# Performance work log

Hardware: AMD Instinct MI355X
Metric: run time of the kernel (lower is better)

## Reference

```python
import jax, jax.numpy as jnp
import numpy as np

B, L, D_MODEL = 2, 1024, 512
N_LAYERS, D_STATE, D_CONV = 6, 16, 4
D_INNER = 2 * D_MODEL          # Mamba default expand=2
DT_RANK = (D_MODEL + 15) // 16  # ceil(d_model/16) = 32
EPS = 1.1920929e-07             # torch RMSNorm default eps (fp32 machine eps)


def rmsnorm(x, w):
    return x * jax.lax.rsqrt(jnp.mean(x * x, axis=-1, keepdims=True) + EPS) * w


def selective_scan(u, dt, A, Bm, Cm, Dv):
    # u, dt: (B,L,E); A: (E,N); Bm, Cm: (B,L,N); Dv: (E,)
    dA = jnp.exp(jnp.einsum('ble,en->blen', dt, A))    # discretized A (ZOH)
    dBu = jnp.einsum('ble,bln->blen', dt * u, Bm)      # discretized B * u (Euler)

    def step(h, inp):
        dA_t, dBu_t, C_t = inp
        h = dA_t * h + dBu_t                           # (B,E,N) state update
        y = jnp.einsum('ben,bn->be', h, C_t)
        return h, y

    h0 = jnp.zeros((u.shape[0], u.shape[2], A.shape[1]), u.dtype)
    _, ys = jax.lax.scan(step, h0,
                         (dA.transpose(1, 0, 2, 3), dBu.transpose(1, 0, 2, 3),
                          Cm.transpose(1, 0, 2)))
    return ys.transpose(1, 0, 2) + u * Dv


def mamba_block(x, p):
    xz = jnp.einsum('bld,ed->ble', x, p['in_proj_w'])  # (B,L,2E)
    xi, z = jnp.split(xz, 2, axis=-1)
    # causal depthwise conv1d (kernel D_CONV) + bias + SiLU
    xc = jnp.pad(xi.transpose(0, 2, 1), ((0, 0), (0, 0), (D_CONV - 1, 0)))
    xc = jax.lax.conv_general_dilated(xc, p['conv_w'][:, None, :], (1,), 'VALID',
                                      feature_group_count=D_INNER)
    xi = jax.nn.silu(xc.transpose(0, 2, 1) + p['conv_b'])
    dbc = jnp.einsum('ble,re->blr', xi, p['x_proj_w'])  # (B,L,R+2N)
    dt, Bm, Cm = jnp.split(dbc, [DT_RANK, DT_RANK + D_STATE], axis=-1)
    dt = jax.nn.softplus(jnp.einsum('blr,er->ble', dt, p['dt_w']) + p['dt_b'])
    y = selective_scan(xi, dt, -jnp.exp(p['A_log']), Bm, Cm, p['D'])
    y = y * jax.nn.silu(z)                              # gate branch
    return jnp.einsum('ble,de->bld', y, p['out_w'])


def setup_inputs() -> dict:
    key = jax.random.key(0)
    ks = jax.random.split(key, 8)
    s = 0.02
    return {
        'x': jax.random.normal(ks[0], (B, L, D_MODEL), jnp.float32),
        'position_embedding': jax.random.normal(ks[1], (B, L, D_MODEL), jnp.float32) * 0.02,
        'norm_w': jnp.ones((D_MODEL,), jnp.float32),
        'in_proj_w': jax.random.normal(ks[2], (N_LAYERS, 2 * D_INNER, D_MODEL), jnp.float32) * s,
        'conv_w': jax.random.normal(ks[3], (N_LAYERS, D_INNER, D_CONV), jnp.float32) * 0.2,
        'conv_b': jnp.zeros((N_LAYERS, D_INNER), jnp.float32),
        'x_proj_w': jax.random.normal(ks[4], (N_LAYERS, DT_RANK + 2 * D_STATE, D_INNER), jnp.float32) * s,
        'dt_w': jax.random.normal(ks[5], (N_LAYERS, D_INNER, DT_RANK), jnp.float32) * s,
        'dt_b': jnp.full((N_LAYERS, D_INNER), -4.6, jnp.float32),  # softplus(dt_b) ~ 0.01
        'A_log': jnp.broadcast_to(
            jnp.log(jnp.arange(1, D_STATE + 1, dtype=jnp.float32)),
            (N_LAYERS, D_INNER, D_STATE)) + jnp.zeros((N_LAYERS, D_INNER, D_STATE), jnp.float32),
        'D': jnp.ones((N_LAYERS, D_INNER), jnp.float32),
        'out_w': jax.random.normal(ks[6], (N_LAYERS, D_MODEL, D_INNER), jnp.float32) * s,
    }


def reference(x, position_embedding, norm_w, in_proj_w, conv_w, conv_b,
              x_proj_w, dt_w, dt_b, A_log, D, out_w):
    stacked = dict(in_proj_w=in_proj_w, conv_w=conv_w, conv_b=conv_b,
                   x_proj_w=x_proj_w, dt_w=dt_w, dt_b=dt_b,
                   A_log=A_log, D=D, out_w=out_w)

    def body(h, p):
        h = h + position_embedding          # added at the start of every layer
        h = mamba_block(rmsnorm(h, norm_w), p)  # NOTE: no residual, per source
        return h, None

    h, _ = jax.lax.scan(body, x, stacked)
    return h
```

## Files before the change

kernel.cpp:

```cpp
#include <hip/hip_runtime.h>
#include <hip/hip_bf16.h>


typedef __attribute__((ext_vector_type(8))) short bf16x8;
typedef __attribute__((ext_vector_type(4))) float f32x4;

__device__ __forceinline__ float bf2f(unsigned short u) {
    unsigned int x = ((unsigned int)u) << 16;
    return __builtin_bit_cast(float, x);
}
__device__ __forceinline__ unsigned short f2bf(float f) {
    __hip_bfloat16 h = __float2bfloat16(f);
    return __builtin_bit_cast(unsigned short, h);
}
__device__ __forceinline__ float ldin(const void* p, size_t i, int isbf) {
    return isbf ? bf2f(((const unsigned short*)p)[i]) : ((const float*)p)[i];
}
__device__ __forceinline__ float softplus_f(float x) {
    return (x > 20.f) ? x : log1pf(__expf(x));
}
__device__ __forceinline__ void split2(float x, unsigned short& h, unsigned short& l) {
    h = f2bf(x);
    l = f2bf(x - bf2f(h));
}

#define S1 (6*2048*512)
#define S2 (6*512*1024)
#define S3 (6*64*1024)
#define S4 (6*1024*32)
__global__ __launch_bounds__(256) void wsplit_all(
    const void* __restrict__ ipw, const void* __restrict__ ow,
    const void* __restrict__ xpw, const void* __restrict__ dtw,
    const void* __restrict__ Dw,
    unsigned short* __restrict__ h1, unsigned short* __restrict__ l1,
    unsigned short* __restrict__ h2, unsigned short* __restrict__ l2,
    unsigned short* __restrict__ h3, unsigned short* __restrict__ l3,
    unsigned short* __restrict__ h4, unsigned short* __restrict__ l4,
    int* __restrict__ flag)
{
    int g = blockIdx.x * 256 + threadIdx.x;
    const int isbf = (*(const unsigned int*)Dw == 0x3F800000u) ? 0 : 1;
    if (g == 0) *flag = isbf;
    const void* src; unsigned short *dh, *dl; int i;
    if (g < S1)                { src = ipw; dh = h1; dl = l1; i = g; }
    else if (g < S1+S2)        { src = ow;  dh = h2; dl = l2; i = g - S1; }
    else if (g < S1+S2+S3)     { src = xpw; dh = h3; dl = l3; i = g - S1 - S2; }
    else if (g < S1+S2+S3+S4)  { src = dtw; dh = h4; dl = l4; i = g - S1 - S2 - S3; }
    else return;
    unsigned short hh, ll;
    split2(ldin(src, i, isbf), hh, ll);
    dh[i] = hh; dl[i] = ll;
}

__global__ __launch_bounds__(256) void gemm128(
    const unsigned short* __restrict__ Ah, const unsigned short* __restrict__ Al,
    int lda,
    const unsigned short* __restrict__ Wh, const unsigned short* __restrict__ Wl,
    long woff,
    float* __restrict__ Cf, int N, int K)
{
    __shared__ __align__(16) unsigned short As[2][128][40];
    __shared__ __align__(16) unsigned short Ws[2][128][40];

    const int m0 = blockIdx.x * 128, n0 = blockIdx.y * 128;
    const int t = threadIdx.x, lane = t & 63, wave = t >> 6;
    const int wm = (wave & 1) * 64, wn = (wave >> 1) * 64;
    const int srow = t >> 1, scol = (t & 1) * 16;

    const unsigned short* ah = Ah + (size_t)(m0 + srow) * lda + scol;
    const unsigned short* al = Al + (size_t)(m0 + srow) * lda + scol;
    const unsigned short* wh = Wh + woff + (size_t)(n0 + srow) * K + scol;
    const unsigned short* wl = Wl + woff + (size_t)(n0 + srow) * K + scol;

    f32x4 acc[4][4] = {};
    const int fm = lane & 15, fk = (lane >> 4) * 8;

    uint4 r0, r1, r2, r3, r4, r5, r6, r7;
#define LD128(K0) do { \
        r0 = *(const uint4*)(ah + (K0));     r1 = *(const uint4*)(ah + (K0) + 8); \
        r2 = *(const uint4*)(al + (K0));     r3 = *(const uint4*)(al + (K0) + 8); \
        r4 = *(const uint4*)(wh + (K0));     r5 = *(const uint4*)(wh + (K0) + 8); \
        r6 = *(const uint4*)(wl + (K0));     r7 = *(const uint4*)(wl + (K0) + 8); \
    } while (0)
#define ST128() do { \
        *(uint4*)(&As[0][srow][scol])     = r0; *(uint4*)(&As[0][srow][scol + 8]) = r1; \
        *(uint4*)(&As[1][srow][scol])     = r2; *(uint4*)(&As[1][srow][scol + 8]) = r3; \
        *(uint4*)(&Ws[0][srow][scol])     = r4; *(uint4*)(&Ws[0][srow][scol + 8]) = r5; \
        *(uint4*)(&Ws[1][srow][scol])     = r6; *(uint4*)(&Ws[1][srow][scol + 8]) = r7; \
    } while (0)

    LD128(0);
    ST128();
    __syncthreads();

    for (int k0 = 0; k0 < K; k0 += 32) {
        const int more = (k0 + 32 < K);
        if (more) LD128(k0 + 32);

        bf16x8 a_h[4], a_l[4], w_h[4], w_l[4];
#pragma unroll
        for (int i = 0; i < 4; ++i) {
            a_h[i] = *(const bf16x8*)(&As[0][wm + i * 16 + fm][fk]);
            a_l[i] = *(const bf16x8*)(&As[1][wm + i * 16 + fm][fk]);
            w_h[i] = *(const bf16x8*)(&Ws[0][wn + i * 16 + fm][fk]);
            w_l[i] = *(const bf16x8*)(&Ws[1][wn + i * 16 + fm][fk]);
        }
#pragma unroll
        for (int mi = 0; mi < 4; ++mi)
#pragma unroll
            for (int ni = 0; ni < 4; ++ni) {
                acc[mi][ni] = __builtin_amdgcn_mfma_f32_16x16x32_bf16(
                    a_h[mi], w_h[ni], acc[mi][ni], 0, 0, 0);
                acc[mi][ni] = __builtin_amdgcn_mfma_f32_16x16x32_bf16(
                    a_h[mi], w_l[ni], acc[mi][ni], 0, 0, 0);
                acc[mi][ni] = __builtin_amdgcn_mfma_f32_16x16x32_bf16(
                    a_l[mi], w_h[ni], acc[mi][ni], 0, 0, 0);
            }

        if (more) {
            __syncthreads();
            ST128();
            __syncthreads();
        }
    }
#undef LD128
#undef ST128

    const int col = lane & 15, rb = (lane >> 4) * 4;
#pragma unroll
    for (int mi = 0; mi < 4; ++mi)
#pragma unroll
        for (int ni = 0; ni < 4; ++ni)
#pragma unroll
            for (int r = 0; r < 4; ++r) {
                int gm = m0 + wm + mi * 16 + rb + r;
                int gn = n0 + wn + ni * 16 + col;
                Cf[(size_t)gm * N + gn] = acc[mi][ni][r];
            }
}

template <int ACT>
__global__ __launch_bounds__(256) void gemm_hl(
    const unsigned short* __restrict__ Ah, const unsigned short* __restrict__ Al,
    int lda,
    const unsigned short* __restrict__ Wh, const unsigned short* __restrict__ Wl,
    long woff,
    float* __restrict__ Cf, long zstride,
    const void* __restrict__ bias, long boff, const int* __restrict__ flag,
    int N, int K, int Kc)
{
    const int isbf = *flag;
    __shared__ __align__(16) unsigned short As[2][64][40];
    __shared__ __align__(16) unsigned short Ws[2][64][40];

    const int m0 = blockIdx.x * 64, n0 = blockIdx.y * 64;
    const int kb = blockIdx.z * Kc;
    const int t = threadIdx.x;
    const int lane = t & 63, wave = t >> 6;
    const int wm = (wave & 1) * 32, wn = (wave >> 1) * 32;
    const int srow = t >> 2, scol = (t & 3) * 8;

    const unsigned short* ah = Ah + (size_t)(m0 + srow) * lda + scol;
    const unsigned short* al = Al + (size_t)(m0 + srow) * lda + scol;
    const unsigned short* wh = Wh + woff + (size_t)(n0 + srow) * K + scol;
    const unsigned short* wl = Wl + woff + (size_t)(n0 + srow) * K + scol;

    f32x4 acc[2][2] = {};

    uint4 r0, r1, r2, r3;
#define LD64(K0) do { \
        r0 = *(const uint4*)(ah + (K0)); \
        r1 = *(const uint4*)(al + (K0)); \
        r2 = *(const uint4*)(wh + (K0)); \
        r3 = *(const uint4*)(wl + (K0)); \
    } while (0)
#define ST64() do { \
        *(uint4*)(&As[0][srow][scol]) = r0; \
        *(uint4*)(&As[1][srow][scol]) = r1; \
        *(uint4*)(&Ws[0][srow][scol]) = r2; \
        *(uint4*)(&Ws[1][srow][scol]) = r3; \
    } while (0)

    LD64(kb);
    ST64();
    __syncthreads();

    for (int k0 = kb; k0 < kb + Kc; k0 += 32) {
        const int more = (k0 + 32 < kb + Kc);
        if (more) LD64(k0 + 32);

        const int fm = lane & 15, fk = (lane >> 4) * 8;
        bf16x8 a0h = *(const bf16x8*)(&As[0][wm + fm][fk]);
        bf16x8 a1h = *(const bf16x8*)(&As[0][wm + 16 + fm][fk]);
        bf16x8 w0h = *(const bf16x8*)(&Ws[0][wn + fm][fk]);
        bf16x8 w1h = *(const bf16x8*)(&Ws[0][wn + 16 + fm][fk]);
        bf16x8 a0l = *(const bf16x8*)(&As[1][wm + fm][fk]);
        bf16x8 a1l = *(const bf16x8*)(&As[1][wm + 16 + fm][fk]);
        bf16x8 w0l = *(const bf16x8*)(&Ws[1][wn + fm][fk]);
        bf16x8 w1l = *(const bf16x8*)(&Ws[1][wn + 16 + fm][fk]);

        acc[0][0] = __builtin_amdgcn_mfma_f32_16x16x32_bf16(a0h, w0h, acc[0][0], 0, 0, 0);
        acc[0][1] = __builtin_amdgcn_mfma_f32_16x16x32_bf16(a0h, w1h, acc[0][1], 0, 0, 0);
        acc[1][0] = __builtin_amdgcn_mfma_f32_16x16x32_bf16(a1h, w0h, acc[1][0], 0, 0, 0);
        acc[1][1] = __builtin_amdgcn_mfma_f32_16x16x32_bf16(a1h, w1h, acc[1][1], 0, 0, 0);
        acc[0][0] = __builtin_amdgcn_mfma_f32_16x16x32_bf16(a0h, w0l, acc[0][0], 0, 0, 0);
        acc[0][1] = __builtin_amdgcn_mfma_f32_16x16x32_bf16(a0h, w1l, acc[0][1], 0, 0, 0);
        acc[1][0] = __builtin_amdgcn_mfma_f32_16x16x32_bf16(a1h, w0l, acc[1][0], 0, 0, 0);
        acc[1][1] = __builtin_amdgcn_mfma_f32_16x16x32_bf16(a1h, w1l, acc[1][1], 0, 0, 0);
        acc[0][0] = __builtin_amdgcn_mfma_f32_16x16x32_bf16(a0l, w0h, acc[0][0], 0, 0, 0);
        acc[0][1] = __builtin_amdgcn_mfma_f32_16x16x32_bf16(a0l, w1h, acc[0][1], 0, 0, 0);
        acc[1][0] = __builtin_amdgcn_mfma_f32_16x16x32_bf16(a1l, w0h, acc[1][0], 0, 0, 0);
        acc[1][1] = __builtin_amdgcn_mfma_f32_16x16x32_bf16(a1l, w1h, acc[1][1], 0, 0, 0);

        if (more) {
            __syncthreads();
            ST64();
            __syncthreads();
        }
    }
#undef LD64
#undef ST64

    float* Cp = Cf + (size_t)blockIdx.z * zstride;
    const int col = lane & 15, rb = (lane >> 4) * 4;
#pragma unroll
    for (int mi = 0; mi < 2; ++mi)
#pragma unroll
        for (int ni = 0; ni < 2; ++ni)
#pragma unroll
            for (int r = 0; r < 4; ++r) {
                int gm = m0 + wm + mi * 16 + rb + r;
                int gn = n0 + wn + ni * 16 + col;
                float v = acc[mi][ni][r];
                if (bias) v += ldin(bias, boff + gn, isbf);
                if (ACT == 1) v = softplus_f(v);
                Cp[(size_t)gm * N + gn] = v;
            }
}

__global__ __launch_bounds__(256) void xp_reduce(
    const float* __restrict__ Pxp, float* __restrict__ dbc,
    unsigned short* __restrict__ dth, unsigned short* __restrict__ dtl)
{
    int g = blockIdx.x * 256 + threadIdx.x;
    float s = 0.f;
#pragma unroll
    for (int z = 0; z < 8; ++z) s += Pxp[(size_t)z * 131072 + g];
    dbc[g] = s;
    int n = g & 63, t = g >> 6;
    if (n < 32) {
        unsigned short hh, ll;
        split2(s, hh, ll);
        dth[t * 32 + n] = hh; dtl[t * 32 + n] = ll;
    }
}

__global__ __launch_bounds__(256) void rmsnorm_k(
    const void* __restrict__ hsrc, int hdyn, const void* __restrict__ pos,
    const void* __restrict__ nw, const int* __restrict__ flag,
    unsigned short* __restrict__ xnh, unsigned short* __restrict__ xnl)
{
    const int isbf = *flag;
    const int row = blockIdx.x;
    const int t = threadIdx.x;
    const size_t base = (size_t)row * 512;
    float h0 = hdyn ? ldin(hsrc, base + t, isbf)       : ((const float*)hsrc)[base + t];
    float h1 = hdyn ? ldin(hsrc, base + 256 + t, isbf) : ((const float*)hsrc)[base + 256 + t];
    float v0 = h0 + ldin(pos, base + t, isbf);
    float v1 = h1 + ldin(pos, base + 256 + t, isbf);
    float ss = v0 * v0 + v1 * v1;
#pragma unroll
    for (int o = 32; o; o >>= 1) ss += __shfl_xor(ss, o, 64);
    __shared__ float sw[4];
    if ((t & 63) == 0) sw[t >> 6] = ss;
    __syncthreads();
    float tot = sw[0] + sw[1] + sw[2] + sw[3];
    float sc = rsqrtf(tot * (1.0f / 512.0f) + 1.1920929e-07f);
    float o0 = v0 * sc * ldin(nw, t, isbf);
    float o1 = v1 * sc * ldin(nw, 256 + t, isbf);
    unsigned short hh, ll;
    split2(o0, hh, ll); xnh[base + t] = hh;       xnl[base + t] = ll;
    split2(o1, hh, ll); xnh[base + 256 + t] = hh; xnl[base + 256 + t] = ll;
}

__global__ __launch_bounds__(256) void conv_silu_k(
    const float* __restrict__ xz,
    const void* __restrict__ cw, long cwoff,
    const void* __restrict__ cb, long cboff,
    const int* __restrict__ flag,
    float* __restrict__ xi,
    unsigned short* __restrict__ xih, unsigned short* __restrict__ xil)
{
    const int isbf = *flag;
    int g = blockIdx.x * 256 + threadIdx.x;
    int e = g & 1023;
    int l = (g >> 10) & 1023;
    int b = g >> 20;
    float acc = ldin(cb, cboff + e, isbf);
#pragma unroll
    for (int k = 0; k < 4; ++k) {
        int ls = l - 3 + k;
        if (ls >= 0)
            acc += ldin(cw, cwoff + e * 4 + k, isbf) *
                   xz[((size_t)(b * 1024 + ls)) * 2048 + e];
    }
    acc = acc / (1.f + __expf(-acc));
    xi[g] = acc;
    unsigned short hh, ll;
    split2(acc, hh, ll);
    xih[g] = hh; xil[g] = ll;
}

#define CL 16
#define NCH 64

__global__ __launch_bounds__(256) void scan_stage1(
    const float* __restrict__ dtp, const float* __restrict__ u,
    const float* __restrict__ dbc,
    const void* __restrict__ alog, long aoff, const int* __restrict__ flag,
    float* __restrict__ P, float* __restrict__ S)
{
    const int isbf = *flag;
    int g = blockIdx.x * 256 + threadIdx.x;
    int e = g & 1023, c = (g >> 10) & (NCH - 1), b = g >> 16;
    int t0 = b * 1024 + c * CL;

    float dv[CL], uv[CL];
#pragma unroll
    for (int i = 0; i < CL; ++i) {
        dv[i] = dtp[(size_t)(t0 + i) * 1024 + e];
        uv[i] = u[(size_t)(t0 + i) * 1024 + e];
    }

    float Aen[16], Pn[16], Sn[16];
#pragma unroll
    for (int n = 0; n < 16; ++n) {
        Aen[n] = -__expf(ldin(alog, aoff + e * 16 + n, isbf));
        Pn[n] = 1.f; Sn[n] = 0.f;
    }
#pragma unroll
    for (int i = 0; i < CL; ++i) {
        float d = dv[i], du = d * uv[i];
        const float4* Bp = (const float4*)(dbc + (size_t)(t0 + i) * 64 + 32);
        float4 b0 = Bp[0], b1 = Bp[1], b2 = Bp[2], b3 = Bp[3];
        float Bt[16] = {b0.x,b0.y,b0.z,b0.w, b1.x,b1.y,b1.z,b1.w,
                        b2.x,b2.y,b2.z,b2.w, b3.x,b3.y,b3.z,b3.w};
#pragma unroll
        for (int n = 0; n < 16; ++n) {
            float a = __expf(d * Aen[n]);
            Sn[n] = a * Sn[n] + du * Bt[n];
            Pn[n] *= a;
        }
    }
    size_t ob = ((size_t)(b * NCH + c) * 16) * 1024 + e;
#pragma unroll
    for (int n = 0; n < 16; ++n) {
        P[ob + (size_t)n * 1024] = Pn[n];
        S[ob + (size_t)n * 1024] = Sn[n];
    }
}

__global__ __launch_bounds__(256) void scan_stage2(
    float* __restrict__ PH, const float* __restrict__ S)
{
    int g = blockIdx.x * 256 + threadIdx.x;
    int e = g & 1023, n = (g >> 10) & 15, b = g >> 14;
    float H = 0.f;
    for (int cb = 0; cb < NCH; cb += 8) {
        float p[8], s[8];
#pragma unroll
        for (int j = 0; j < 8; ++j) {
            size_t idx = ((size_t)(b * NCH + cb + j) * 16 + n) * 1024 + e;
            p[j] = PH[idx]; s[j] = S[idx];
        }
#pragma unroll
        for (int j = 0; j < 8; ++j) {
            size_t idx = ((size_t)(b * NCH + cb + j) * 16 + n) * 1024 + e;
            PH[idx] = H;
            H = p[j] * H + s[j];
        }
    }
}

__global__ __launch_bounds__(256) void scan_stage3(
    const float* __restrict__ dtp, const float* __restrict__ u,
    const float* __restrict__ dbc,
    const void* __restrict__ alog, long aoff,
    const void* __restrict__ Dv, long doff,
    const int* __restrict__ flag,
    const float* __restrict__ xz, const float* __restrict__ H0,
    unsigned short* __restrict__ yh, unsigned short* __restrict__ yl)
{
    const int isbf = *flag;
    int g = blockIdx.x * 256 + threadIdx.x;
    int e = g & 1023, c = (g >> 10) & (NCH - 1), b = g >> 16;
    int t0 = b * 1024 + c * CL;

    float dv[CL], uv[CL], zv[CL];
#pragma unroll
    for (int i = 0; i < CL; ++i) {
        dv[i] = dtp[(size_t)(t0 + i) * 1024 + e];
        uv[i] = u[(size_t)(t0 + i) * 1024 + e];
        zv[i] = xz[(size_t)(t0 + i) * 2048 + 1024 + e];
    }

    float Aen[16], h[16];
    size_t ob = ((size_t)(b * NCH + c) * 16) * 1024 + e;
#pragma unroll
    for (int n = 0; n < 16; ++n) {
        Aen[n] = -__expf(ldin(alog, aoff + e * 16 + n, isbf));
        h[n] = H0[ob + (size_t)n * 1024];
    }
    float De = ldin(Dv, doff + e, isbf);
#pragma unroll
    for (int i = 0; i < CL; ++i) {
        float d = dv[i], uu = uv[i], du = d * uu;
        const float4* Bp = (const float4*)(dbc + (size_t)(t0 + i) * 64 + 32);
        float4 b0 = Bp[0], b1 = Bp[1], b2 = Bp[2], b3 = Bp[3];
        float4 c0 = Bp[4], c1 = Bp[5], c2 = Bp[6], c3 = Bp[7];
        float Bt[16] = {b0.x,b0.y,b0.z,b0.w, b1.x,b1.y,b1.z,b1.w,
                        b2.x,b2.y,b2.z,b2.w, b3.x,b3.y,b3.z,b3.w};
        float Ct[16] = {c0.x,c0.y,c0.z,c0.w, c1.x,c1.y,c1.z,c1.w,
                        c2.x,c2.y,c2.z,c2.w, c3.x,c3.y,c3.z,c3.w};
        float y = 0.f;
#pragma unroll
        for (int n = 0; n < 16; ++n) {
            float a = __expf(d * Aen[n]);
            h[n] = a * h[n] + du * Bt[n];
            y += h[n] * Ct[n];
        }
        float sz = zv[i] / (1.f + __expf(-zv[i]));
        float yv = (y + uu * De) * sz;
        unsigned short hh, ll;
        split2(yv, hh, ll);
        yh[(size_t)(t0 + i) * 1024 + e] = hh;
        yl[(size_t)(t0 + i) * 1024 + e] = ll;
    }
}

extern "C" void kernel_launch(void* const* d_in, const int* in_sizes, int n_in,
                              void* d_out, int out_size, void* d_ws, size_t ws_size,
                              hipStream_t stream)
{
    const void* x    = d_in[0];
    const void* pos  = d_in[1];
    const void* nw   = d_in[2];
    const void* ipw  = d_in[3];
    const void* cw   = d_in[4];
    const void* cb   = d_in[5];
    const void* xpw  = d_in[6];
    const void* dtw  = d_in[7];
    const void* dtb  = d_in[8];
    const void* alog = d_in[9];
    const void* Dw   = d_in[10];
    const void* ow   = d_in[11];

    char* w = (char*)d_ws;
    auto take = [&](size_t bytes) { char* p = w; w += (bytes + 255) & ~255ull; return p; };

    float* h    = (float*)take(2048ull * 512 * 4);
    float* xz   = (float*)take(2048ull * 2048 * 4);
    float* xi   = (float*)take(2048ull * 1024 * 4);
    float* dtf  = (float*)take(2048ull * 1024 * 4);
    float* dbc  = (float*)take(2048ull * 64 * 4);
    float* P    = (float*)take(2ull * NCH * 16 * 1024 * 4);
    float* S    = (float*)take(2ull * NCH * 16 * 1024 * 4);
    float* Pxp  = (float*)take(8ull * 2048 * 64 * 4);
    unsigned short* xnh = (unsigned short*)take(2048ull * 512 * 2);
    unsigned short* xnl = (unsigned short*)take(2048ull * 512 * 2);
    unsigned short* xih = (unsigned short*)take(2048ull * 1024 * 2);
    unsigned short* xil = (unsigned short*)take(2048ull * 1024 * 2);
    unsigned short* yh  = (unsigned short*)take(2048ull * 1024 * 2);
    unsigned short* yl  = (unsigned short*)take(2048ull * 1024 * 2);
    unsigned short* dth = (unsigned short*)take(2048ull * 32 * 2);
    unsigned short* dtl = (unsigned short*)take(2048ull * 32 * 2);
    unsigned short* wip_h = (unsigned short*)take(6ull * 2048 * 512 * 2);
    unsigned short* wip_l = (unsigned short*)take(6ull * 2048 * 512 * 2);
    unsigned short* wow_h = (unsigned short*)take(6ull * 512 * 1024 * 2);
    unsigned short* wow_l = (unsigned short*)take(6ull * 512 * 1024 * 2);
    unsigned short* wxp_h = (unsigned short*)take(6ull * 64 * 1024 * 2);
    unsigned short* wxp_l = (unsigned short*)take(6ull * 64 * 1024 * 2);
    unsigned short* wdt_h = (unsigned short*)take(6ull * 1024 * 32 * 2);
    unsigned short* wdt_l = (unsigned short*)take(6ull * 1024 * 32 * 2);
    int* flag = (int*)take(256);

    wsplit_all<<<(S1 + S2 + S3 + S4 + 255) / 256, 256, 0, stream>>>(
        ipw, ow, xpw, dtw, Dw,
        wip_h, wip_l, wow_h, wow_l, wxp_h, wxp_l, wdt_h, wdt_l, flag);

    for (int l = 0; l < 6; ++l) {
        rmsnorm_k<<<2048, 256, 0, stream>>>(
            l == 0 ? x : (const void*)h, l == 0 ? 1 : 0, pos, nw, flag, xnh, xnl);
        gemm128<<<dim3(16, 16), 256, 0, stream>>>(
            xnh, xnl, 512, wip_h, wip_l, (long)l * 2048 * 512, xz, 2048, 512);
        conv_silu_k<<<8192, 256, 0, stream>>>(xz, cw, (long)l * 4096, cb, (long)l * 1024,
                                              flag, xi, xih, xil);
        gemm_hl<0><<<dim3(32, 1, 8), 256, 0, stream>>>(
            xih, xil, 1024, wxp_h, wxp_l, (long)l * 64 * 1024,
            Pxp, 2048l * 64, nullptr, 0, flag, 64, 1024, 128);
        xp_reduce<<<512, 256, 0, stream>>>(Pxp, dbc, dth, dtl);
        gemm_hl<1><<<dim3(32, 16), 256, 0, stream>>>(
            dth, dtl, 32, wdt_h, wdt_l, (long)l * 1024 * 32,
            dtf, 0, dtb, (long)l * 1024, flag, 1024, 32, 32);
        scan_stage1<<<512, 256, 0, stream>>>(dtf, xi, dbc, alog, (long)l * 16384,
                                             flag, P, S);
        scan_stage2<<<128, 256, 0, stream>>>(P, S);
        scan_stage3<<<512, 256, 0, stream>>>(dtf, xi, dbc, alog, (long)l * 16384,
                                             Dw, (long)l * 1024, flag, xz, P, yh, yl);
        float* outp = (l < 5) ? h : (float*)d_out;
        gemm_hl<0><<<dim3(32, 8), 256, 0, stream>>>(
            yh, yl, 1024, wow_h, wow_l, (long)l * 512 * 1024,
            outp, 0, nullptr, 0, flag, 512, 1024, 1024);
    }
}
```

Before: 845.2 us.

## Fuse x_proj reduction, dt projection and scan stage1; derive chunk decay from dt sum

Merges the split-K reduction of x_proj, the dt_proj GEMM with softplus, and the first chunked-scan stage into one kernel. The 32-wide dt projection is now computed in fp32 from shared memory, so the bf16 hi/lo split of dt weights and the separate GEMM launch go away. Stage1 no longer writes the per-chunk decay product P. It stores the chunk sum of dt instead, and stage2 recomputes the decay as exp(A*sum dt), which cuts global traffic. The cost is redundant reduction work across the four e-groups and an extra exp per element in stage2.

Measured after the change: 835.5 us. No clear change (-1.1%).

```diff
diff --git a/kernel.cpp b/kernel.cpp
--- a/kernel.cpp
+++ b/kernel.cpp
@@ -27,15 +27,12 @@
 #define S1 (6*2048*512)
 #define S2 (6*512*1024)
 #define S3 (6*64*1024)
-#define S4 (6*1024*32)
 __global__ __launch_bounds__(256) void wsplit_all(
     const void* __restrict__ ipw, const void* __restrict__ ow,
-    const void* __restrict__ xpw, const void* __restrict__ dtw,
-    const void* __restrict__ Dw,
+    const void* __restrict__ xpw, const void* __restrict__ Dw,
     unsigned short* __restrict__ h1, unsigned short* __restrict__ l1,
     unsigned short* __restrict__ h2, unsigned short* __restrict__ l2,
     unsigned short* __restrict__ h3, unsigned short* __restrict__ l3,
-    unsigned short* __restrict__ h4, unsigned short* __restrict__ l4,
     int* __restrict__ flag)
 {
     int g = blockIdx.x * 256 + threadIdx.x;
@@ -45,7 +42,6 @@
     if (g < S1)                { src = ipw; dh = h1; dl = l1; i = g; }
     else if (g < S1+S2)        { src = ow;  dh = h2; dl = l2; i = g - S1; }
     else if (g < S1+S2+S3)     { src = xpw; dh = h3; dl = l3; i = g - S1 - S2; }
-    else if (g < S1+S2+S3+S4)  { src = dtw; dh = h4; dl = l4; i = g - S1 - S2 - S3; }
     else return;
     unsigned short hh, ll;
     split2(ldin(src, i, isbf), hh, ll);
@@ -238,23 +234,6 @@
             }
 }
 
-__global__ __launch_bounds__(256) void xp_reduce(
-    const float* __restrict__ Pxp, float* __restrict__ dbc,
-    unsigned short* __restrict__ dth, unsigned short* __restrict__ dtl)
-{
-    int g = blockIdx.x * 256 + threadIdx.x;
-    float s = 0.f;
-#pragma unroll
-    for (int z = 0; z < 8; ++z) s += Pxp[(size_t)z * 131072 + g];
-    dbc[g] = s;
-    int n = g & 63, t = g >> 6;
-    if (n < 32) {
-        unsigned short hh, ll;
-        split2(s, hh, ll);
-        dth[t * 32 + n] = hh; dtl[t * 32 + n] = ll;
-    }
-}
-
 __global__ __launch_bounds__(256) void rmsnorm_k(
     const void* __restrict__ hsrc, int hdyn, const void* __restrict__ pos,
     const void* __restrict__ nw, const int* __restrict__ flag,
@@ -314,34 +293,69 @@
 #define CL 16
 #define NCH 64
 
-__global__ __launch_bounds__(256) void scan_stage1(
-    const float* __restrict__ dtp, const float* __restrict__ u,
-    const float* __restrict__ dbc,
-    const void* __restrict__ alog, long aoff, const int* __restrict__ flag,
-    float* __restrict__ P, float* __restrict__ S)
+__global__ __launch_bounds__(256) void xp_dt_scan1(
+    const float* __restrict__ Pxp,
+    const void* __restrict__ dtw, long dtwoff,
+    const void* __restrict__ dtb, long dtboff,
+    const void* __restrict__ alog, long aoff,
+    const float* __restrict__ xi,
+    const int* __restrict__ flag,
+    float* __restrict__ dbc, float* __restrict__ dtf,
+    float* __restrict__ S, float* __restrict__ Dsum)
 {
     const int isbf = *flag;
-    int g = blockIdx.x * 256 + threadIdx.x;
-    int e = g & 1023, c = (g >> 10) & (NCH - 1), b = g >> 16;
-    int t0 = b * 1024 + c * CL;
-
-    float dv[CL], uv[CL];
+    const int tid = threadIdx.x;
+    const int c = blockIdx.x, eg = blockIdx.y, b = blockIdx.z;
+    const int t0 = b * 1024 + c * CL;
+
+    __shared__ float red[CL][64];
+
+    for (int idx = tid; idx < CL * 64; idx += 256) {
+        int ti = idx >> 6, n = idx & 63;
+        float s = 0.f;
+#pragma unroll
+        for (int z = 0; z < 8; ++z)
+            s += Pxp[(size_t)z * 131072 + (size_t)(t0 + ti) * 64 + n];
+        red[ti][n] = s;
+        if (eg == 0) dbc[(size_t)(t0 + ti) * 64 + n] = s;
+    }
+    __syncthreads();
+
+    const int e = eg * 256 + tid;
+
+    float wrow[32];
+#pragma unroll
+    for (int k = 0; k < 32; ++k) wrow[k] = ldin(dtw, dtwoff + (size_t)e * 32 + k, isbf);
+    const float bias = ldin(dtb, dtboff + e, isbf);
+
+    float dv[CL];
 #pragma unroll
     for (int i = 0; i < CL; ++i) {
-        dv[i] = dtp[(size_t)(t0 + i) * 1024 + e];
-        uv[i] = u[(size_t)(t0 + i) * 1024 + e];
-    }
-
-    float Aen[16], Pn[16], Sn[16];
+        const float4* rp = (const float4*)&red[i][0];
+        float acc = bias;
+#pragma unroll
+        for (int k4 = 0; k4 < 8; ++k4) {
+            float4 r4 = rp[k4];
+            acc += r4.x * wrow[k4 * 4 + 0] + r4.y * wrow[k4 * 4 + 1]
+                 + r4.z * wrow[k4 * 4 + 2] + r4.w * wrow[k4 * 4 + 3];
+        }
+        dv[i] = softplus_f(acc);
+        dtf[(size_t)(t0 + i) * 1024 + e] = dv[i];
+    }
+
+    float Aen[16], Sn[16];
 #pragma unroll
     for (int n = 0; n < 16; ++n) {
-        Aen[n] = -__expf(ldin(alog, aoff + e * 16 + n, isbf));
-        Pn[n] = 1.f; Sn[n] = 0.f;
-    }
+        Aen[n] = -__expf(ldin(alog, aoff + (size_t)e * 16 + n, isbf));
+        Sn[n] = 0.f;
+    }
+    float ds = 0.f;
 #pragma unroll
     for (int i = 0; i < CL; ++i) {
-        float d = dv[i], du = d * uv[i];
-        const float4* Bp = (const float4*)(dbc + (size_t)(t0 + i) * 64 + 32);
+        float d = dv[i];
+        ds += d;
+        float du = d * xi[(size_t)(t0 + i) * 1024 + e];
+        const float4* Bp = (const float4*)&red[i][32];
         float4 b0 = Bp[0], b1 = Bp[1], b2 = Bp[2], b3 = Bp[3];
         float Bt[16] = {b0.x,b0.y,b0.z,b0.w, b1.x,b1.y,b1.z,b1.w,
                         b2.x,b2.y,b2.z,b2.w, b3.x,b3.y,b3.z,b3.w};
@@ -349,35 +363,37 @@
         for (int n = 0; n < 16; ++n) {
             float a = __expf(d * Aen[n]);
             Sn[n] = a * Sn[n] + du * Bt[n];
-            Pn[n] *= a;
         }
     }
     size_t ob = ((size_t)(b * NCH + c) * 16) * 1024 + e;
 #pragma unroll
-    for (int n = 0; n < 16; ++n) {
-        P[ob + (size_t)n * 1024] = Pn[n];
-        S[ob + (size_t)n * 1024] = Sn[n];
-    }
+    for (int n = 0; n < 16; ++n) S[ob + (size_t)n * 1024] = Sn[n];
+    Dsum[(size_t)(b * NCH + c) * 1024 + e] = ds;
 }
 
 __global__ __launch_bounds__(256) void scan_stage2(
-    float* __restrict__ PH, const float* __restrict__ S)
-{
+    const float* __restrict__ S, const float* __restrict__ Dsum,
+    const void* __restrict__ alog, long aoff, const int* __restrict__ flag,
+    float* __restrict__ H0)
+{
+    const int isbf = *flag;
     int g = blockIdx.x * 256 + threadIdx.x;
     int e = g & 1023, n = (g >> 10) & 15, b = g >> 14;
+    const float Aen = -__expf(ldin(alog, aoff + (size_t)e * 16 + n, isbf));
     float H = 0.f;
     for (int cb = 0; cb < NCH; cb += 8) {
-        float p[8], s[8];
+        float s[8], pj[8];
 #pragma unroll
         for (int j = 0; j < 8; ++j) {
             size_t idx = ((size_t)(b * NCH + cb + j) * 16 + n) * 1024 + e;
-            p[j] = PH[idx]; s[j] = S[idx];
+            s[j] = S[idx];
+            pj[j] = __expf(Dsum[(size_t)(b * NCH + cb + j) * 1024 + e] * Aen);
         }
 #pragma unroll
         for (int j = 0; j < 8; ++j) {
             size_t idx = ((size_t)(b * NCH + cb + j) * 16 + n) * 1024 + e;
-            PH[idx] = H;
-            H = p[j] * H + s[j];
+            H0[idx] = H;
+            H = pj[j] * H + s[j];
         }
     }
 }
@@ -408,7 +424,7 @@
     size_t ob = ((size_t)(b * NCH + c) * 16) * 1024 + e;
 #pragma unroll
     for (int n = 0; n < 16; ++n) {
-        Aen[n] = -__expf(ldin(alog, aoff + e * 16 + n, isbf));
+        Aen[n] = -__expf(ldin(alog, aoff + (size_t)e * 16 + n, isbf));
         h[n] = H0[ob + (size_t)n * 1024];
     }
     float De = ldin(Dv, doff + e, isbf);
@@ -463,8 +479,9 @@
     float* xi   = (float*)take(2048ull * 1024 * 4);
     float* dtf  = (float*)take(2048ull * 1024 * 4);
     float* dbc  = (float*)take(2048ull * 64 * 4);
-    float* P    = (float*)take(2ull * NCH * 16 * 1024 * 4);
     float* S    = (float*)take(2ull * NCH * 16 * 1024 * 4);
+    float* H0   = (float*)take(2ull * NCH * 16 * 1024 * 4);
+    float* Dsum = (float*)take(2ull * NCH * 1024 * 4);
     float* Pxp  = (float*)take(8ull * 2048 * 64 * 4);
     unsigned short* xnh = (unsigned short*)take(2048ull * 512 * 2);
     unsigned short* xnl = (unsigned short*)take(2048ull * 512 * 2);
@@ -472,21 +489,17 @@
     unsigned short* xil = (unsigned short*)take(2048ull * 1024 * 2);
     unsigned short* yh  = (unsigned short*)take(2048ull * 1024 * 2);
     unsigned short* yl  = (unsigned short*)take(2048ull * 1024 * 2);
-    unsigned short* dth = (unsigned short*)take(2048ull * 32 * 2);
-    unsigned short* dtl = (unsigned short*)take(2048ull * 32 * 2);
     unsigned short* wip_h = (unsigned short*)take(6ull * 2048 * 512 * 2);
     unsigned short* wip_l = (unsigned short*)take(6ull * 2048 * 512 * 2);
     unsigned short* wow_h = (unsigned short*)take(6ull * 512 * 1024 * 2);
     unsigned short* wow_l = (unsigned short*)take(6ull * 512 * 1024 * 2);
     unsigned short* wxp_h = (unsigned short*)take(6ull * 64 * 1024 * 2);
     unsigned short* wxp_l = (unsigned short*)take(6ull * 64 * 1024 * 2);
-    unsigned short* wdt_h = (unsigned short*)take(6ull * 1024 * 32 * 2);
-    unsigned short* wdt_l = (unsigned short*)take(6ull * 1024 * 32 * 2);
     int* flag = (int*)take(256);
 
-    wsplit_all<<<(S1 + S2 + S3 + S4 + 255) / 256, 256, 0, stream>>>(
-        ipw, ow, xpw, dtw, Dw,
-        wip_h, wip_l, wow_h, wow_l, wxp_h, wxp_l, wdt_h, wdt_l, flag);
+    wsplit_all<<<(S1 + S2 + S3 + 255) / 256, 256, 0, stream>>>(
+        ipw, ow, xpw, Dw,
+        wip_h, wip_l, wow_h, wow_l, wxp_h, wxp_l, flag);
 
     for (int l = 0; l < 6; ++l) {
         rmsnorm_k<<<2048, 256, 0, stream>>>(
@@ -498,15 +511,12 @@
         gemm_hl<0><<<dim3(32, 1, 8), 256, 0, stream>>>(
             xih, xil, 1024, wxp_h, wxp_l, (long)l * 64 * 1024,
             Pxp, 2048l * 64, nullptr, 0, flag, 64, 1024, 128);
-        xp_reduce<<<512, 256, 0, stream>>>(Pxp, dbc, dth, dtl);
-        gemm_hl<1><<<dim3(32, 16), 256, 0, stream>>>(
-            dth, dtl, 32, wdt_h, wdt_l, (long)l * 1024 * 32,
-            dtf, 0, dtb, (long)l * 1024, flag, 1024, 32, 32);
-        scan_stage1<<<512, 256, 0, stream>>>(dtf, xi, dbc, alog, (long)l * 16384,
-                                             flag, P, S);
-        scan_stage2<<<128, 256, 0, stream>>>(P, S);
+        xp_dt_scan1<<<dim3(NCH, 4, 2), 256, 0, stream>>>(
+            Pxp, dtw, (long)l * 1024 * 32, dtb, (long)l * 1024,
+            alog, (long)l * 16384, xi, flag, dbc, dtf, S, Dsum);
+        scan_stage2<<<128, 256, 0, stream>>>(S, Dsum, alog, (long)l * 16384, flag, H0);
         scan_stage3<<<512, 256, 0, stream>>>(dtf, xi, dbc, alog, (long)l * 16384,
-                                             Dw, (long)l * 1024, flag, xz, P, yh, yl);
+                                             Dw, (long)l * 1024, flag, xz, H0, yh, yl);
         float* outp = (l < 5) ? h : (float*)d_out;
         gemm_hl<0><<<dim3(32, 8), 256, 0, stream>>>(
             yh, yl, 1024, wow_h, wow_l, (long)l * 512 * 1024,
```
